# Kernel optimization log

Measured on AMD Instinct MI355X. Metric: run time of the kernel, lower is better.

The kernel has to match this reference:

```python
import jax, jax.numpy as jnp
import numpy as np

SIGMAS = [1.0, 2.0, 4.0, 8.0, 16.0]
EPS = 0.05
ITERS = 30
N, M, D = 8192, 8192, 128


def _sqdist(X, Y):
    # ||x_i - y_j||^2, [n, m]
    d2 = (jnp.sum(X * X, axis=1)[:, None]
          + jnp.sum(Y * Y, axis=1)[None, :]
          - 2.0 * (X @ Y.T))
    return jnp.maximum(d2, 0.0)


def _ms_rbf(X, Y):
    d2 = _sqdist(X, Y)
    K = jnp.zeros_like(d2)
    for s in SIGMAS:  # small fixed loop over scales
        K = K + jnp.exp(-d2 / (2.0 * s * s))
    return K / float(len(SIGMAS))


def _sinkhorn_uniform(cost, eps, iters):
    n, m = cost.shape
    dtype = cost.dtype
    log_a = jnp.asarray(-np.log(float(n)), dtype)
    log_b = jnp.asarray(-np.log(float(m)), dtype)
    log_K = -(cost - jax.lax.stop_gradient(jnp.min(cost))) / eps

    def step(carry, _):
        log_u, log_v = carry
        log_u = log_a - jax.scipy.special.logsumexp(log_K + log_v[None, :], axis=1)
        log_v = log_b - jax.scipy.special.logsumexp(log_K + log_u[:, None], axis=0)
        return (log_u, log_v), None

    init = (jnp.zeros((n,), dtype), jnp.zeros((m,), dtype))
    (log_u, log_v), _ = jax.lax.scan(step, init, None, length=iters)
    return jnp.exp(log_u[:, None] + log_K + log_v[None, :])


def setup_inputs() -> dict:
    key = jax.random.key(0)
    kx, ky = jax.random.split(key)
    X = jax.random.normal(kx, (N, D), dtype=jnp.float32)
    Y = jax.random.normal(ky, (M, D), dtype=jnp.float32)
    return {"X": X, "Y": Y}


def reference(X, Y):
    Kxx = jnp.mean(_ms_rbf(X, X))
    Kyy = jnp.mean(_ms_rbf(Y, Y))
    Kxy = _ms_rbf(X, Y)
    cost = 1.0 / float(X.shape[0] * Y.shape[0]) - Kxy
    Gamma = _sinkhorn_uniform(cost, EPS, ITERS)
    Kxy_weighted = jnp.sum(Gamma * Kxy)
    return Kxx + Kyy - 2.0 * Kxy_weighted
```

## Files before the change

### kernel.cpp

```cpp
#include <hip/hip_runtime.h>
#include <math.h>

#define NR 8192
#define DDIM 128

static constexpr float LOG_AB2 = -13.0f;
static constexpr float OFF2    = -28.853900817779268f;
static constexpr float C8      = 0.11315255222658537f;
static constexpr float DQK8    = 1.0f / 255.0f;
static constexpr float E1 = -0.7213475204444817f;
static constexpr float E2 = -0.18033688011112043f;
static constexpr float E3 = -0.045084220027780107f;
static constexpr float E4 = -0.011271055006945027f;
static constexpr float E5 = -0.0028177637517362567f;

typedef __attribute__((ext_vector_type(8))) _Float16 f16x8;
typedef __attribute__((ext_vector_type(4))) float    f32x4;

#if defined(__has_builtin)
#if __has_builtin(__builtin_amdgcn_exp2f)
#define EX2_IMPL(x) __builtin_amdgcn_exp2f(x)
#endif
#endif
#ifndef EX2_IMPL
extern "C" __device__ float __ocml_native_exp2_f32(float);
#define EX2_IMPL(x) __ocml_native_exp2_f32(x)
#endif
__device__ inline float ex2(float x) { return EX2_IMPL(x); }

typedef const unsigned int __attribute__((address_space(1)))* gas_ptr;
typedef unsigned int __attribute__((address_space(3)))*       las_ptr;
__device__ inline void gload16(const void* g, void* l) {
    __builtin_amdgcn_global_load_lds((gas_ptr)g, (las_ptr)l, 16, 0, 0);
}

__device__ inline unsigned short f2h(float f) {
    return __builtin_bit_cast(unsigned short, (_Float16)f);
}

__global__ __launch_bounds__(256) void convh_k(const float* __restrict__ X,
                                               unsigned short* __restrict__ H) {
    const int i = blockIdx.x * 1024 + threadIdx.x * 4;
    const float4 v = *reinterpret_cast<const float4*>(&X[i]);
    ushort4 h;
    h.x = f2h(v.x);
    h.y = f2h(v.y);
    h.z = f2h(v.z);
    h.w = f2h(v.w);
    *reinterpret_cast<ushort4*>(&H[i]) = h;
}

__global__ __launch_bounds__(256) void rownorm_k(const float* __restrict__ X,
                                                 float* __restrict__ nrm) {
    const int lane = threadIdx.x & 63;
    const int w    = threadIdx.x >> 6;
    const int row  = blockIdx.x * 4 + w;
    const float2 v = *reinterpret_cast<const float2*>(&X[(size_t)row * DDIM + lane * 2]);
    float s = v.x * v.x + v.y * v.y;
#pragma unroll
    for (int off = 32; off; off >>= 1) s += __shfl_xor(s, off);
    if (lane == 0) nrm[row] = s;
}

template <int MODE>
__global__ __launch_bounds__(256) void gemm_mfma_k(const unsigned short* __restrict__ XF,
                                                   const unsigned short* __restrict__ YF,
                                                   const float* __restrict__ nxp,
                                                   const float* __restrict__ nyp,
                                                   unsigned char* __restrict__ K8,
                                                   double* __restrict__ sums) {
    int bm, bn;
    const unsigned short *A, *B;
    const float *na, *nb;
    if (MODE == 0) {
        bm = blockIdx.x; bn = blockIdx.y;
        A = XF; B = YF; na = nxp; nb = nyp;
    } else {
        const int lin = blockIdx.x;
        int i = (int)((129.0f - sqrtf(16641.0f - 8.0f * (float)lin)) * 0.5f);
        while (i * 64 - i * (i - 1) / 2 > lin) --i;
        while ((i + 1) * 64 - (i + 1) * i / 2 <= lin) ++i;
        bm = i;
        bn = i + (lin - (i * 64 - i * (i - 1) / 2));
        const int sel = blockIdx.y;
        A = B = sel ? YF : XF;
        na = nb = sel ? nyp : nxp;
    }
    __shared__ unsigned short Tile[128 * 64];

    const int t    = threadIdx.x;
    const int lane = t & 63;
    const int w    = t >> 6;
    const int wr   = w >> 1, wc = w & 1;
    const int l15  = lane & 15, lg = lane >> 4;

    const int lr = lane >> 3;
    const int u  = (lane & 7) ^ lr;
    const int ss = u & 3;

    f32x4 acc[4][4];
#pragma unroll
    for (int mi = 0; mi < 4; ++mi)
#pragma unroll
        for (int ni = 0; ni < 4; ++ni) acc[mi][ni] = (f32x4){0.f, 0.f, 0.f, 0.f};

    const unsigned short* src = (u < 4)
        ? A + (size_t)(bm * 128 + lr) * DDIM + ss * 8
        : B + (size_t)(bn * 128 + lr) * DDIM + ss * 8;

    for (int kc = 0; kc < 4; ++kc) {
        if (kc) __syncthreads();
        const int ko = kc * 32;
#pragma unroll
        for (int c = 0; c < 4; ++c) {
            const int row0 = w * 32 + c * 8;
            gload16(src + (size_t)row0 * DDIM + ko, &Tile[row0 * 64]);
        }
        __syncthreads();

        f16x8 bf[4];
#pragma unroll
        for (int ni = 0; ni < 4; ++ni) {
            const int R = wc * 64 + ni * 16 + l15;
            bf[ni] = *reinterpret_cast<const f16x8*>(&Tile[R * 64 + ((4 + lg) ^ (R & 7)) * 8]);
        }
#pragma unroll
        for (int mi = 0; mi < 4; ++mi) {
            const int R = wr * 64 + mi * 16 + l15;
            const f16x8 af = *reinterpret_cast<const f16x8*>(&Tile[R * 64 + (lg ^ (R & 7)) * 8]);
#pragma unroll
            for (int ni = 0; ni < 4; ++ni)
                acc[mi][ni] = __builtin_amdgcn_mfma_f32_16x16x32_f16(af, bf[ni], acc[mi][ni], 0, 0, 0);
        }
    }

    const int mBase = bm * 128 + wr * 64;
    const int nBase = bn * 128 + wc * 64;
    float nbv[4];
#pragma unroll
    for (int ni = 0; ni < 4; ++ni) nbv[ni] = nb[nBase + ni * 16 + l15];

    if (MODE == 0) {
#pragma unroll
        for (int mi = 0; mi < 4; ++mi) {
#pragma unroll
            for (int j = 0; j < 4; ++j) {
                const int m = mBase + mi * 16 + lg * 4 + j;
                const float nav = na[m];
                unsigned char* krow = &K8[(size_t)m * NR + nBase + l15];
#pragma unroll
                for (int ni = 0; ni < 4; ++ni) {
                    float d2 = fmaf(-2.f, acc[mi][ni][j], nav + nbv[ni]);
                    d2 = fmaxf(d2, 0.f);
                    const float kv = 0.2f * (ex2(d2 * E1) + ex2(d2 * E2) + ex2(d2 * E3) +
                                             ex2(d2 * E4) + ex2(d2 * E5));
                    krow[ni * 16] = (unsigned char)__float2uint_rn(kv * 255.f);
                }
            }
        }
    } else {
        double lsum = 0.0;
#pragma unroll
        for (int mi = 0; mi < 4; ++mi) {
#pragma unroll
            for (int j = 0; j < 4; ++j) {
                const int m = mBase + mi * 16 + lg * 4 + j;
                const float nav = na[m];
                float rs = 0.f;
#pragma unroll
                for (int ni = 0; ni < 4; ++ni) {
                    float d2 = fmaf(-2.f, acc[mi][ni][j], nav + nbv[ni]);
                    d2 = fmaxf(d2, 0.f);
                    rs += 0.2f * (ex2(d2 * E1) + ex2(d2 * E2) + ex2(d2 * E3) +
                                  ex2(d2 * E4) + ex2(d2 * E5));
                }
                lsum += (double)rs;
            }
        }
        if (bn > bm) lsum *= 2.0;
#pragma unroll
        for (int o = 32; o; o >>= 1) lsum += __shfl_xor(lsum, o);
        if (lane == 0) atomicAdd(&sums[1 + blockIdx.y], lsum);
    }
}

__global__ __launch_bounds__(256) void init_lv_k(float* __restrict__ log_v) {
    log_v[blockIdx.x * 256 + threadIdx.x] = OFF2;
}

__global__ __launch_bounds__(256) void sink_row_k(const unsigned char* __restrict__ K8,
                                                  const float* __restrict__ log_v,
                                                  float* __restrict__ log_u) {
    __shared__ float red[4][8];
    const int t  = threadIdx.x;
    const int r0 = blockIdx.x * 8;
    const float4* Lv4 = reinterpret_cast<const float4*>(log_v);
    float s[8];
#pragma unroll
    for (int r = 0; r < 8; ++r) s[r] = 0.f;
#pragma unroll
    for (int p = 0; p < 2; ++p) {
        const int g = t + p * 256;
        const float4 l0 = Lv4[4 * g + 0];
        const float4 l1 = Lv4[4 * g + 1];
        const float4 l2 = Lv4[4 * g + 2];
        const float4 l3 = Lv4[4 * g + 3];
        const float lvv[16] = {l0.x, l0.y, l0.z, l0.w, l1.x, l1.y, l1.z, l1.w,
                               l2.x, l2.y, l2.z, l2.w, l3.x, l3.y, l3.z, l3.w};
        const uint4* col = reinterpret_cast<const uint4*>(K8 + (size_t)r0 * NR) + g;
#pragma unroll
        for (int r = 0; r < 8; ++r) {
            const uint4 wq = col[(size_t)r * 512];
            const unsigned wd[4] = {wq.x, wq.y, wq.z, wq.w};
#pragma unroll
            for (int d = 0; d < 4; ++d) {
                const unsigned a = wd[d];
                s[r] += ex2(fmaf((float)(a & 255u),          C8, lvv[4 * d + 0]))
                      + ex2(fmaf((float)((a >> 8) & 255u),   C8, lvv[4 * d + 1]))
                      + ex2(fmaf((float)((a >> 16) & 255u),  C8, lvv[4 * d + 2]))
                      + ex2(fmaf((float)(a >> 24),           C8, lvv[4 * d + 3]));
            }
        }
    }
    const int lane = t & 63, wv = t >> 6;
#pragma unroll
    for (int r = 0; r < 8; ++r) {
        float v = s[r];
#pragma unroll
        for (int o = 32; o; o >>= 1) v += __shfl_xor(v, o);
        if (lane == 0) red[wv][r] = v;
    }
    __syncthreads();
    if (t < 8) {
        const float stot = (red[0][t] + red[1][t]) + (red[2][t] + red[3][t]);
        log_u[r0 + t] = LOG_AB2 - __log2f(stot) + OFF2;
    }
}

__global__ __launch_bounds__(256) void sink_colp_k(const unsigned char* __restrict__ K8,
                                                   const float* __restrict__ log_u,
                                                   float* __restrict__ ps) {
    const int t   = threadIdx.x;
    const int cg4 = blockIdx.x * 256 + t;
    const int rc  = blockIdx.y;
    const uint4* base = reinterpret_cast<const uint4*>(K8) + (size_t)rc * 32 * 512 + cg4;
    const float* lu = log_u + rc * 32;
    float s16[16];
#pragma unroll
    for (int e = 0; e < 16; ++e) s16[e] = 0.f;
#pragma unroll 4
    for (int r = 0; r < 32; ++r) {
        const uint4 wq = base[(size_t)r * 512];
        const float lur = lu[r];
        const unsigned wd[4] = {wq.x, wq.y, wq.z, wq.w};
#pragma unroll
        for (int d = 0; d < 4; ++d) {
            const unsigned a = wd[d];
            s16[4 * d + 0] += ex2(fmaf((float)(a & 255u),         C8, lur));
            s16[4 * d + 1] += ex2(fmaf((float)((a >> 8) & 255u),  C8, lur));
            s16[4 * d + 2] += ex2(fmaf((float)((a >> 16) & 255u), C8, lur));
            s16[4 * d + 3] += ex2(fmaf((float)(a >> 24),          C8, lur));
        }
    }
    float4* pv = reinterpret_cast<float4*>(ps + (size_t)rc * NR + cg4 * 16);
#pragma unroll
    for (int d = 0; d < 4; ++d)
        pv[d] = {s16[4 * d + 0], s16[4 * d + 1], s16[4 * d + 2], s16[4 * d + 3]};
}

__global__ __launch_bounds__(256) void sink_combine_k(const float* __restrict__ ps,
                                                      float* __restrict__ log_v) {
    __shared__ float red[4][64];
    const int lane = threadIdx.x & 63;
    const int grp  = threadIdx.x >> 6;
    const int col  = blockIdx.x * 64 + lane;
    float s = 0.f;
#pragma unroll 8
    for (int c = grp * 64; c < grp * 64 + 64; ++c) s += ps[(size_t)c * NR + col];
    red[grp][lane] = s;
    __syncthreads();
    if (grp == 0) {
        const float stot = (red[0][lane] + red[1][lane]) + (red[2][lane] + red[3][lane]);
        log_v[col] = LOG_AB2 - __log2f(stot) + OFF2;
    }
}

__global__ __launch_bounds__(256) void gamma_sum_k(const unsigned char* __restrict__ K8,
                                                   const float* __restrict__ log_u,
                                                   const float* __restrict__ log_v,
                                                   double* __restrict__ S) {
    const int t   = threadIdx.x;
    const int cg4 = blockIdx.x * 256 + t;
    const int rc  = blockIdx.y;
    float lvp[16];
#pragma unroll
    for (int e = 0; e < 16; ++e) lvp[e] = log_v[cg4 * 16 + e] - OFF2;
    const uint4* base = reinterpret_cast<const uint4*>(K8) + (size_t)rc * 32 * 512 + cg4;
    const float* lu = log_u + rc * 32;
    double acc = 0.0;
#pragma unroll 4
    for (int r = 0; r < 32; ++r) {
        const uint4 w = base[(size_t)r * 512];
        const float lur = lu[r];
        const unsigned wd[4] = {w.x, w.y, w.z, w.w};
        float rs = 0.f;
#pragma unroll
        for (int d = 0; d < 4; ++d) {
            const unsigned a = wd[d];
            const float q0 = (float)(a & 255u);
            const float q1 = (float)((a >> 8) & 255u);
            const float q2 = (float)((a >> 16) & 255u);
            const float q3 = (float)(a >> 24);
            rs = fmaf(ex2(fmaf(q0, C8, lur + lvp[4 * d + 0])), q0, rs);
            rs = fmaf(ex2(fmaf(q1, C8, lur + lvp[4 * d + 1])), q1, rs);
            rs = fmaf(ex2(fmaf(q2, C8, lur + lvp[4 * d + 2])), q2, rs);
            rs = fmaf(ex2(fmaf(q3, C8, lur + lvp[4 * d + 3])), q3, rs);
        }
        acc += (double)rs;
    }
#pragma unroll
    for (int o = 32; o; o >>= 1) acc += __shfl_xor(acc, o);
    if ((t & 63) == 0) atomicAdd(S, acc);
}

__global__ void finalize_k(const double* __restrict__ scal, float* __restrict__ out) {
    const double inv = 1.0 / (8192.0 * 8192.0);
    out[0] = (float)(scal[1] * inv + scal[2] * inv - 2.0 * (double)DQK8 * scal[3]);
}

extern "C" void kernel_launch(void* const* d_in, const int* in_sizes, int n_in,
                              void* d_out, int out_size, void* d_ws, size_t ws_size,
                              hipStream_t stream) {
    const float* X = (const float*)d_in[0];
    const float* Y = (const float*)d_in[1];

    char* ws = (char*)d_ws;
    unsigned char* K8 = (unsigned char*)ws;
    float* nx    = (float*)(ws + 67108864);
    float* ny    = nx + NR;
    float* log_u = ny + NR;
    float* log_v = log_u + NR;
    char*  scal  = (char*)(log_v + NR);
    double* scal_d = (double*)scal;
    float* ps = (float*)(scal + 512);
    unsigned short* XF = (unsigned short*)(ws + 75629056);
    unsigned short* YF = XF + NR * DDIM;
    const size_t needed = 75629056 + 2 * (size_t)NR * DDIM * 2;
    if (ws_size < needed) return;

    (void)hipMemsetAsync(scal, 0, 512, stream);

    convh_k<<<NR * DDIM / 1024, 256, 0, stream>>>(X, XF);
    convh_k<<<NR * DDIM / 1024, 256, 0, stream>>>(Y, YF);
    rownorm_k<<<NR / 4, 256, 0, stream>>>(X, nx);
    rownorm_k<<<NR / 4, 256, 0, stream>>>(Y, ny);

    gemm_mfma_k<0><<<dim3(64, 64), 256, 0, stream>>>(XF, YF, nx, ny, K8, scal_d);
    gemm_mfma_k<1><<<dim3(2080, 2), 256, 0, stream>>>(XF, YF, nx, ny, nullptr, scal_d);

    init_lv_k<<<NR / 256, 256, 0, stream>>>(log_v);

    for (int it = 0; it < 30; ++it) {
        sink_row_k<<<NR / 8, 256, 0, stream>>>(K8, log_v, log_u);
        sink_colp_k<<<dim3(2, 256), 256, 0, stream>>>(K8, log_u, ps);
        sink_combine_k<<<128, 256, 0, stream>>>(ps, log_v);
    }

    gamma_sum_k<<<dim3(2, 256), 256, 0, stream>>>(K8, log_u, log_v, scal_d + 3);
    finalize_k<<<1, 1, 0, stream>>>(scal_d, (float*)d_out);
}
```

Before: 1.572 ms.

## Load full K-depth GEMM tiles once and process 16 rows per Sinkhorn row block

The MFMA GEMM now stages the whole 128-deep A and B tiles into shared memory (64KB) with a single barrier, instead of four 32-deep chunks with repeated syncs. The XOR swizzle moves to 16 columns to match the wider rows. Separately, the Sinkhorn row kernel handles 16 rows per block rather than 8, so each log_v load is reused across more rows and half as many blocks are launched. The cost is more LDS and registers per block, which lowers occupancy in both kernels.

Result: slower. 1.673 ms (+6.4%).

```diff
diff --git a/kernel.cpp b/kernel.cpp
--- a/kernel.cpp
+++ b/kernel.cpp
@@ -86,7 +86,8 @@
         A = B = sel ? YF : XF;
         na = nb = sel ? nyp : nxp;
     }
-    __shared__ unsigned short Tile[128 * 64];
+    __shared__ unsigned short As[128 * 128];
+    __shared__ unsigned short Bs[128 * 128];
 
     const int t    = threadIdx.x;
     const int lane = t & 63;
@@ -94,9 +95,8 @@
     const int wr   = w >> 1, wc = w & 1;
     const int l15  = lane & 15, lg = lane >> 4;
 
-    const int lr = lane >> 3;
-    const int u  = (lane & 7) ^ lr;
-    const int ss = u & 3;
+    const int r4 = lane >> 4;
+    const int p  = lane & 15;
 
     f32x4 acc[4][4];
 #pragma unroll
@@ -104,30 +104,27 @@
 #pragma unroll
         for (int ni = 0; ni < 4; ++ni) acc[mi][ni] = (f32x4){0.f, 0.f, 0.f, 0.f};
 
-    const unsigned short* src = (u < 4)
-        ? A + (size_t)(bm * 128 + lr) * DDIM + ss * 8
-        : B + (size_t)(bn * 128 + lr) * DDIM + ss * 8;
-
-    for (int kc = 0; kc < 4; ++kc) {
-        if (kc) __syncthreads();
-        const int ko = kc * 32;
-#pragma unroll
-        for (int c = 0; c < 4; ++c) {
-            const int row0 = w * 32 + c * 8;
-            gload16(src + (size_t)row0 * DDIM + ko, &Tile[row0 * 64]);
-        }
-        __syncthreads();
-
+#pragma unroll
+    for (int c = 0; c < 8; ++c) {
+        const int rloc = w * 32 + c * 4 + r4;
+        const int u    = p ^ (rloc & 15);
+        gload16(A + (size_t)(bm * 128 + rloc) * DDIM + u * 8, &As[(w * 32 + c * 4) * 128]);
+        gload16(B + (size_t)(bn * 128 + rloc) * DDIM + u * 8, &Bs[(w * 32 + c * 4) * 128]);
+    }
+    __syncthreads();
+
+#pragma unroll
+    for (int ks = 0; ks < 4; ++ks) {
         f16x8 bf[4];
 #pragma unroll
         for (int ni = 0; ni < 4; ++ni) {
             const int R = wc * 64 + ni * 16 + l15;
-            bf[ni] = *reinterpret_cast<const f16x8*>(&Tile[R * 64 + ((4 + lg) ^ (R & 7)) * 8]);
+            bf[ni] = *reinterpret_cast<const f16x8*>(&Bs[R * 128 + ((ks * 4 + lg) ^ l15) * 8]);
         }
 #pragma unroll
         for (int mi = 0; mi < 4; ++mi) {
             const int R = wr * 64 + mi * 16 + l15;
-            const f16x8 af = *reinterpret_cast<const f16x8*>(&Tile[R * 64 + (lg ^ (R & 7)) * 8]);
+            const f16x8 af = *reinterpret_cast<const f16x8*>(&As[R * 128 + ((ks * 4 + lg) ^ l15) * 8]);
 #pragma unroll
             for (int ni = 0; ni < 4; ++ni)
                 acc[mi][ni] = __builtin_amdgcn_mfma_f32_16x16x32_f16(af, bf[ni], acc[mi][ni], 0, 0, 0);
@@ -191,16 +188,16 @@
 __global__ __launch_bounds__(256) void sink_row_k(const unsigned char* __restrict__ K8,
                                                   const float* __restrict__ log_v,
                                                   float* __restrict__ log_u) {
-    __shared__ float red[4][8];
+    __shared__ float red[4][16];
     const int t  = threadIdx.x;
-    const int r0 = blockIdx.x * 8;
+    const int r0 = blockIdx.x * 16;
     const float4* Lv4 = reinterpret_cast<const float4*>(log_v);
-    float s[8];
-#pragma unroll
-    for (int r = 0; r < 8; ++r) s[r] = 0.f;
-#pragma unroll
-    for (int p = 0; p < 2; ++p) {
-        const int g = t + p * 256;
+    float s[16];
+#pragma unroll
+    for (int r = 0; r < 16; ++r) s[r] = 0.f;
+#pragma unroll
+    for (int pp = 0; pp < 2; ++pp) {
+        const int g = t + pp * 256;
         const float4 l0 = Lv4[4 * g + 0];
         const float4 l1 = Lv4[4 * g + 1];
         const float4 l2 = Lv4[4 * g + 2];
@@ -209,7 +206,7 @@
                                l2.x, l2.y, l2.z, l2.w, l3.x, l3.y, l3.z, l3.w};
         const uint4* col = reinterpret_cast<const uint4*>(K8 + (size_t)r0 * NR) + g;
 #pragma unroll
-        for (int r = 0; r < 8; ++r) {
+        for (int r = 0; r < 16; ++r) {
             const uint4 wq = col[(size_t)r * 512];
             const unsigned wd[4] = {wq.x, wq.y, wq.z, wq.w};
 #pragma unroll
@@ -224,14 +221,14 @@
     }
     const int lane = t & 63, wv = t >> 6;
 #pragma unroll
-    for (int r = 0; r < 8; ++r) {
+    for (int r = 0; r < 16; ++r) {
         float v = s[r];
 #pragma unroll
         for (int o = 32; o; o >>= 1) v += __shfl_xor(v, o);
         if (lane == 0) red[wv][r] = v;
     }
     __syncthreads();
-    if (t < 8) {
+    if (t < 16) {
         const float stot = (red[0][t] + red[1][t]) + (red[2][t] + red[3][t]);
         log_u[r0 + t] = LOG_AB2 - __log2f(stot) + OFF2;
     }
@@ -361,7 +358,7 @@
     init_lv_k<<<NR / 256, 256, 0, stream>>>(log_v);
 
     for (int it = 0; it < 30; ++it) {
-        sink_row_k<<<NR / 8, 256, 0, stream>>>(K8, log_v, log_u);
+        sink_row_k<<<NR / 16, 256, 0, stream>>>(K8, log_v, log_u);
         sink_colp_k<<<dim3(2, 256), 256, 0, stream>>>(K8, log_u, ps);
         sink_combine_k<<<128, 256, 0, stream>>>(ps, log_v);
     }
```

## Swap MFMA operands for packed 4-byte K8 stores; replace atomics with block partial sums

Applied to the files above, without the earlier changes.

Swapping the A/B operands of the MFMA transposes the accumulator layout, so each lane holds four consecutive columns of one row. The MODE 0 epilogue can then pack four 8-bit kernel values into one 32-bit store instead of issuing scattered byte stores. The symmetric-sum MODE 1 path now writes one double per block into a buffer, and a new single-block kernel reduces those values instead of using per-wave double atomics. This makes the reduction deterministic and removes atomic contention, at the cost of one extra launch and reusing the ps buffer as scratch.

Result: faster. 1.424 ms (-9.4%).

```diff
diff --git a/kernel.cpp b/kernel.cpp
--- a/kernel.cpp
+++ b/kernel.cpp
@@ -68,7 +68,7 @@
                                                    const float* __restrict__ nxp,
                                                    const float* __restrict__ nyp,
                                                    unsigned char* __restrict__ K8,
-                                                   double* __restrict__ sums) {
+                                                   double* __restrict__ bsum) {
     int bm, bn;
     const unsigned short *A, *B;
     const float *na, *nb;
@@ -87,6 +87,7 @@
         na = nb = sel ? nyp : nxp;
     }
     __shared__ unsigned short Tile[128 * 64];
+    __shared__ double redd[4];
 
     const int t    = threadIdx.x;
     const int lane = t & 63;
@@ -130,46 +131,48 @@
             const f16x8 af = *reinterpret_cast<const f16x8*>(&Tile[R * 64 + (lg ^ (R & 7)) * 8]);
 #pragma unroll
             for (int ni = 0; ni < 4; ++ni)
-                acc[mi][ni] = __builtin_amdgcn_mfma_f32_16x16x32_f16(af, bf[ni], acc[mi][ni], 0, 0, 0);
+                acc[mi][ni] = __builtin_amdgcn_mfma_f32_16x16x32_f16(bf[ni], af, acc[mi][ni], 0, 0, 0);
         }
     }
 
     const int mBase = bm * 128 + wr * 64;
     const int nBase = bn * 128 + wc * 64;
-    float nbv[4];
-#pragma unroll
-    for (int ni = 0; ni < 4; ++ni) nbv[ni] = nb[nBase + ni * 16 + l15];
+    float nav[4];
+#pragma unroll
+    for (int mi = 0; mi < 4; ++mi) nav[mi] = na[mBase + mi * 16 + l15];
 
     if (MODE == 0) {
 #pragma unroll
-        for (int mi = 0; mi < 4; ++mi) {
-#pragma unroll
-            for (int j = 0; j < 4; ++j) {
-                const int m = mBase + mi * 16 + lg * 4 + j;
-                const float nav = na[m];
-                unsigned char* krow = &K8[(size_t)m * NR + nBase + l15];
-#pragma unroll
-                for (int ni = 0; ni < 4; ++ni) {
-                    float d2 = fmaf(-2.f, acc[mi][ni][j], nav + nbv[ni]);
+        for (int ni = 0; ni < 4; ++ni) {
+            const float4 nb4 = *reinterpret_cast<const float4*>(&nb[nBase + ni * 16 + lg * 4]);
+            const float nbj[4] = {nb4.x, nb4.y, nb4.z, nb4.w};
+#pragma unroll
+            for (int mi = 0; mi < 4; ++mi) {
+                const int m = mBase + mi * 16 + l15;
+                unsigned o = 0;
+#pragma unroll
+                for (int j = 0; j < 4; ++j) {
+                    float d2 = fmaf(-2.f, acc[mi][ni][j], nav[mi] + nbj[j]);
                     d2 = fmaxf(d2, 0.f);
                     const float kv = 0.2f * (ex2(d2 * E1) + ex2(d2 * E2) + ex2(d2 * E3) +
                                              ex2(d2 * E4) + ex2(d2 * E5));
-                    krow[ni * 16] = (unsigned char)__float2uint_rn(kv * 255.f);
+                    o |= (unsigned)(unsigned char)__float2uint_rn(kv * 255.f) << (8 * j);
                 }
+                *reinterpret_cast<unsigned*>(&K8[(size_t)m * NR + nBase + ni * 16 + lg * 4]) = o;
             }
         }
     } else {
         double lsum = 0.0;
 #pragma unroll
-        for (int mi = 0; mi < 4; ++mi) {
-#pragma unroll
-            for (int j = 0; j < 4; ++j) {
-                const int m = mBase + mi * 16 + lg * 4 + j;
-                const float nav = na[m];
+        for (int ni = 0; ni < 4; ++ni) {
+            const float4 nb4 = *reinterpret_cast<const float4*>(&nb[nBase + ni * 16 + lg * 4]);
+            const float nbj[4] = {nb4.x, nb4.y, nb4.z, nb4.w};
+#pragma unroll
+            for (int mi = 0; mi < 4; ++mi) {
                 float rs = 0.f;
 #pragma unroll
-                for (int ni = 0; ni < 4; ++ni) {
-                    float d2 = fmaf(-2.f, acc[mi][ni][j], nav + nbv[ni]);
+                for (int j = 0; j < 4; ++j) {
+                    float d2 = fmaf(-2.f, acc[mi][ni][j], nav[mi] + nbj[j]);
                     d2 = fmaxf(d2, 0.f);
                     rs += 0.2f * (ex2(d2 * E1) + ex2(d2 * E2) + ex2(d2 * E3) +
                                   ex2(d2 * E4) + ex2(d2 * E5));
@@ -180,7 +183,28 @@
         if (bn > bm) lsum *= 2.0;
 #pragma unroll
         for (int o = 32; o; o >>= 1) lsum += __shfl_xor(lsum, o);
-        if (lane == 0) atomicAdd(&sums[1 + blockIdx.y], lsum);
+        if (lane == 0) redd[w] = lsum;
+        __syncthreads();
+        if (t == 0)
+            bsum[(size_t)blockIdx.y * 2080 + blockIdx.x] =
+                (redd[0] + redd[1]) + (redd[2] + redd[3]);
+    }
+}
+
+__global__ __launch_bounds__(256) void reduce_sums_k(const double* __restrict__ bsum,
+                                                     double* __restrict__ scal_d) {
+    __shared__ double red[8];
+    const int t = threadIdx.x, lane = t & 63, w = t >> 6;
+#pragma unroll
+    for (int half = 0; half < 2; ++half) {
+        double s = 0.0;
+        for (int i = t; i < 2080; i += 256) s += bsum[half * 2080 + i];
+#pragma unroll
+        for (int o = 32; o; o >>= 1) s += __shfl_xor(s, o);
+        if (lane == 0) red[w] = s;
+        __syncthreads();
+        if (t == 0) scal_d[1 + half] = (red[0] + red[1]) + (red[2] + red[3]);
+        __syncthreads();
     }
 }
 
@@ -343,6 +367,7 @@
     char*  scal  = (char*)(log_v + NR);
     double* scal_d = (double*)scal;
     float* ps = (float*)(scal + 512);
+    double* bsum = (double*)ps;
     unsigned short* XF = (unsigned short*)(ws + 75629056);
     unsigned short* YF = XF + NR * DDIM;
     const size_t needed = 75629056 + 2 * (size_t)NR * DDIM * 2;
@@ -355,8 +380,9 @@
     rownorm_k<<<NR / 4, 256, 0, stream>>>(X, nx);
     rownorm_k<<<NR / 4, 256, 0, stream>>>(Y, ny);
 
-    gemm_mfma_k<0><<<dim3(64, 64), 256, 0, stream>>>(XF, YF, nx, ny, K8, scal_d);
-    gemm_mfma_k<1><<<dim3(2080, 2), 256, 0, stream>>>(XF, YF, nx, ny, nullptr, scal_d);
+    gemm_mfma_k<0><<<dim3(64, 64), 256, 0, stream>>>(XF, YF, nx, ny, K8, nullptr);
+    gemm_mfma_k<1><<<dim3(2080, 2), 256, 0, stream>>>(XF, YF, nx, ny, nullptr, bsum);
+    reduce_sums_k<<<1, 256, 0, stream>>>(bsum, scal_d);
 
     init_lv_k<<<NR / 256, 256, 0, stream>>>(log_v);
 
```
